# Kernel optimization log

Measured on AMD Instinct MI355X. Metric: run time of the kernel, lower is better.

The kernel has to match this reference:

```python
import jax, jax.numpy as jnp
import numpy as np

B_, T_, IN_, H_, N_ = 16, 4096, 2, 256, 256
TWO_PI = 6.283185307179586


def setup_inputs() -> dict:
    key = jax.random.key(0)
    ks = jax.random.split(key, 12)
    x = jax.random.normal(ks[0], (B_, T_, IN_), dtype=jnp.float32)
    lengths = jax.random.randint(ks[1], (B_,), 1, T_ + 1)  # in [1, T]
    # canonical LRU param init (ring init for eigenvalues)
    u1 = jax.random.uniform(ks[2], (N_,))
    u2 = jax.random.uniform(ks[3], (N_,))
    nu_log = jnp.log(-0.5 * jnp.log(u1 * 0.75 + 0.25))          # |lam| in [0.5, 1)
    theta_log = jnp.log(u2 * TWO_PI + 1e-4)
    B_re = jax.random.normal(ks[4], (N_, IN_)) / np.sqrt(2 * IN_)
    B_im = jax.random.normal(ks[5], (N_, IN_)) / np.sqrt(2 * IN_)
    C_re = jax.random.normal(ks[6], (H_, N_)) / np.sqrt(N_)
    C_im = jax.random.normal(ks[7], (H_, N_)) / np.sqrt(N_)
    D = jax.random.normal(ks[8], (H_, IN_))
    Wh = jax.random.normal(ks[9], (1, H_)) / np.sqrt(H_)
    bh = jnp.zeros((1,), dtype=jnp.float32)
    return {"x": x, "lengths": lengths, "nu_log": nu_log.astype(jnp.float32),
            "theta_log": theta_log.astype(jnp.float32), "B_re": B_re.astype(jnp.float32),
            "B_im": B_im.astype(jnp.float32), "C_re": C_re.astype(jnp.float32),
            "C_im": C_im.astype(jnp.float32), "D": D.astype(jnp.float32),
            "Wh": Wh.astype(jnp.float32), "bh": bh}


def _combine(e1, e2):
    a1, b1 = e1
    a2, b2 = e2
    return a1 * a2, a2 * b1 + b2


def reference(x, lengths, nu_log, theta_log, B_re, B_im, C_re, C_im, D, Wh, bh):
    B, T, _ = x.shape
    lam = jnp.exp(-jnp.exp(nu_log) + 1j * jnp.exp(theta_log))          # [N] complex
    gamma = jnp.sqrt(1.0 - jnp.abs(lam) ** 2)                           # [N] real
    Bmat = (B_re + 1j * B_im) * gamma[:, None]                          # [N, IN]
    Bu = jnp.einsum('bti,ni->btn', x.astype(jnp.complex64), Bmat)       # [B,T,N]
    a = jnp.broadcast_to(lam.astype(jnp.complex64), Bu.shape)
    # parallel associative scan of x_t = lam*x_{t-1} + Bu_t along time
    _, states = jax.lax.associative_scan(_combine, (a, Bu), axis=1)     # [B,T,N]
    C = C_re + 1j * C_im                                                # [H,N]
    y = jnp.einsum('btn,hn->bth', states, C).real + x @ D.T             # [B,T,H]
    mask = (jnp.arange(T) < lengths[:, None])[..., None]                # [B,T,1]
    y = y * mask
    last = jnp.take_along_axis(y, (lengths - 1)[:, None, None], axis=1)[:, 0, :]  # [B,H]
    return last @ Wh.T + bh                                             # [B,1]
```

## Files before the change

kernel.cpp:

```cpp
#include <hip/hip_runtime.h>
#include <hip/hip_bf16.h>

#define B_ 16
#define T_ 4096
#define IN_ 2
#define H_ 256
#define N_ 256

#define TWO_PI_F 6.28318530717958647692f
#define INV_TWO_PI_D 0.15915494309189533576888376337251

__global__ __launch_bounds__(256) void cw_kernel(const float* __restrict__ C_re,
                                                 const float* __restrict__ C_im,
                                                 const float* __restrict__ Wh,
                                                 float2* __restrict__ Cw) {
    int n = blockIdx.x;
    int h = threadIdx.x;
    float w = Wh[h];
    float vr = w * C_re[h * N_ + n];
    float vi = w * C_im[h * N_ + n];
    for (int off = 32; off > 0; off >>= 1) {
        vr += __shfl_down(vr, off);
        vi += __shfl_down(vi, off);
    }
    __shared__ float2 sred[4];
    int wid = threadIdx.x >> 6;
    int lane = threadIdx.x & 63;
    if (lane == 0) sred[wid] = make_float2(vr, vi);
    __syncthreads();
    if (threadIdx.x == 0) {
        float2 t = sred[0];
        t.x += sred[1].x + sred[2].x + sred[3].x;
        t.y += sred[1].y + sred[2].y + sred[3].y;
        Cw[n] = t;
    }
}

__global__ __launch_bounds__(256) void lru_state_kernel(
        const float* __restrict__ x, const int* __restrict__ lengths,
        const float* __restrict__ nu_log, const float* __restrict__ theta_log,
        const float* __restrict__ B_re, const float* __restrict__ B_im,
        const float2* __restrict__ Cw, float* __restrict__ g) {
    const int n = blockIdx.x;
    const int b = blockIdx.y;
    const int L = lengths[b];
    const int tstar = L - 1;

    const float nu = __expf(nu_log[n]);
    const float th = __expf(theta_log[n]);
    const double threv = (double)th * INV_TWO_PI_D;

    const float2* xb = ((const float2*)x) + (size_t)b * T_;

    float a0r = 0.f, a0i = 0.f, a1r = 0.f, a1i = 0.f;
    for (int s = threadIdx.x; s < L; s += 256) {
        int k = tstar - s;
        double f = (double)k * threv;
        float r = (float)(f - rint(f));
        float ang = r * TWO_PI_F;
        float sn, cs;
        __sincosf(ang, &sn, &cs);
        float e = __expf(-(float)k * nu);
        float vr = e * cs;
        float vi = e * sn;
        float2 xv = xb[s];
        a0r = fmaf(vr, xv.x, a0r);
        a0i = fmaf(vi, xv.x, a0i);
        a1r = fmaf(vr, xv.y, a1r);
        a1i = fmaf(vi, xv.y, a1i);
    }

    for (int off = 32; off > 0; off >>= 1) {
        a0r += __shfl_down(a0r, off);
        a0i += __shfl_down(a0i, off);
        a1r += __shfl_down(a1r, off);
        a1i += __shfl_down(a1i, off);
    }
    __shared__ float4 sred[4];
    int wid = threadIdx.x >> 6;
    int lane = threadIdx.x & 63;
    if (lane == 0) sred[wid] = make_float4(a0r, a0i, a1r, a1i);
    __syncthreads();
    if (threadIdx.x == 0) {
        float4 t = sred[0];
        t.x += sred[1].x + sred[2].x + sred[3].x;
        t.y += sred[1].y + sred[2].y + sred[3].y;
        t.z += sred[1].z + sred[2].z + sred[3].z;
        t.w += sred[1].w + sred[2].w + sred[3].w;
        float gamma = sqrtf(1.f - __expf(-2.f * nu));
        float br0 = B_re[2 * n] * gamma, bi0 = B_im[2 * n] * gamma;
        float br1 = B_re[2 * n + 1] * gamma, bi1 = B_im[2 * n + 1] * gamma;
        float str = t.x * br0 - t.y * bi0 + t.z * br1 - t.w * bi1;
        float sti = t.x * bi0 + t.y * br0 + t.z * bi1 + t.w * br1;
        float2 cw = Cw[n];
        g[b * N_ + n] = str * cw.x - sti * cw.y;
    }
}

__global__ __launch_bounds__(256) void out_kernel(
        const float* __restrict__ g, const float* __restrict__ x,
        const int* __restrict__ lengths, const float* __restrict__ D,
        const float* __restrict__ Wh, const float* __restrict__ bh,
        float* __restrict__ out) {
    int b = blockIdx.x;
    int tstar = lengths[b] - 1;
    int h = threadIdx.x;
    float2 xv = ((const float2*)x)[(size_t)b * T_ + tstar];
    float v = g[b * N_ + h] + Wh[h] * (D[2 * h] * xv.x + D[2 * h + 1] * xv.y);
    for (int off = 32; off > 0; off >>= 1) v += __shfl_down(v, off);
    __shared__ float sred[4];
    int wid = threadIdx.x >> 6;
    int lane = threadIdx.x & 63;
    if (lane == 0) sred[wid] = v;
    __syncthreads();
    if (threadIdx.x == 0) {
        out[b] = sred[0] + sred[1] + sred[2] + sred[3] + bh[0];
    }
}

extern "C" void kernel_launch(void* const* d_in, const int* in_sizes, int n_in,
                              void* d_out, int out_size, void* d_ws, size_t ws_size,
                              hipStream_t stream) {
    const float* x         = (const float*)d_in[0];
    const int*   lengths   = (const int*)d_in[1];
    const float* nu_log    = (const float*)d_in[2];
    const float* theta_log = (const float*)d_in[3];
    const float* B_re      = (const float*)d_in[4];
    const float* B_im      = (const float*)d_in[5];
    const float* C_re      = (const float*)d_in[6];
    const float* C_im      = (const float*)d_in[7];
    const float* D         = (const float*)d_in[8];
    const float* Wh        = (const float*)d_in[9];
    const float* bh        = (const float*)d_in[10];
    float* out = (float*)d_out;

    float2* Cw = (float2*)d_ws;
    float*  g  = (float*)d_ws + 2 * N_;

    cw_kernel<<<N_, 256, 0, stream>>>(C_re, C_im, Wh, Cw);
    lru_state_kernel<<<dim3(N_, B_), 256, 0, stream>>>(x, lengths, nu_log, theta_log,
                                                       B_re, B_im, Cw, g);
    out_kernel<<<B_, 256, 0, stream>>>(g, x, lengths, D, Wh, bh, out);
}
```

Baseline: 86.70 us.

## Replace per-step sincos/exp with a complex power recurrence and fuse the output kernel

Each thread now evaluates sincos and exp only twice: once for its starting power lam^k0 and once for the stride factor lam^256. It then advances the power by complex multiplication instead of recomputing the double-precision angle reduction, sincos and exp on every timestep. The output reduction kernel is removed: the D term and bias are written by an extended setup kernel, and each state block adds its contribution to out with an atomic add, saving one launch. The costs are rounding error that accumulates through the recurrence (about 16 steps per thread), order-dependent float atomics, and a dependence on setup_kernel writing out before lru_kernel runs.

```diff
diff --git a/kernel.cpp b/kernel.cpp
--- a/kernel.cpp
+++ b/kernel.cpp
@@ -10,41 +10,57 @@
 #define TWO_PI_F 6.28318530717958647692f
 #define INV_TWO_PI_D 0.15915494309189533576888376337251
 
-__global__ __launch_bounds__(256) void cw_kernel(const float* __restrict__ C_re,
-                                                 const float* __restrict__ C_im,
-                                                 const float* __restrict__ Wh,
-                                                 float2* __restrict__ Cw) {
-    int n = blockIdx.x;
+__global__ __launch_bounds__(256) void setup_kernel(
+        const float* __restrict__ C_re, const float* __restrict__ C_im,
+        const float* __restrict__ Wh, const float* __restrict__ bh,
+        const float* __restrict__ D, const float* __restrict__ x,
+        const int* __restrict__ lengths,
+        float2* __restrict__ Cw, float* __restrict__ out) {
+    __shared__ float2 sred[4];
     int h = threadIdx.x;
-    float w = Wh[h];
-    float vr = w * C_re[h * N_ + n];
-    float vi = w * C_im[h * N_ + n];
-    for (int off = 32; off > 0; off >>= 1) {
-        vr += __shfl_down(vr, off);
-        vi += __shfl_down(vi, off);
-    }
-    __shared__ float2 sred[4];
     int wid = threadIdx.x >> 6;
     int lane = threadIdx.x & 63;
-    if (lane == 0) sred[wid] = make_float2(vr, vi);
-    __syncthreads();
-    if (threadIdx.x == 0) {
-        float2 t = sred[0];
-        t.x += sred[1].x + sred[2].x + sred[3].x;
-        t.y += sred[1].y + sred[2].y + sred[3].y;
-        Cw[n] = t;
+    float w = Wh[h];
+
+    if (blockIdx.x < N_) {
+        int n = blockIdx.x;
+        float vr = w * C_re[h * N_ + n];
+        float vi = w * C_im[h * N_ + n];
+        for (int off = 32; off > 0; off >>= 1) {
+            vr += __shfl_down(vr, off);
+            vi += __shfl_down(vi, off);
+        }
+        if (lane == 0) sred[wid] = make_float2(vr, vi);
+        __syncthreads();
+        if (threadIdx.x == 0) {
+            float2 t = sred[0];
+            t.x += sred[1].x + sred[2].x + sred[3].x;
+            t.y += sred[1].y + sred[2].y + sred[3].y;
+            Cw[n] = t;
+        }
+    } else {
+        int b = blockIdx.x - N_;
+        int tstar = lengths[b] - 1;
+        float2 xv = ((const float2*)x)[(size_t)b * T_ + tstar];
+        float v = w * (D[2 * h] * xv.x + D[2 * h + 1] * xv.y);
+        for (int off = 32; off > 0; off >>= 1) v += __shfl_down(v, off);
+        if (lane == 0) sred[wid] = make_float2(v, 0.f);
+        __syncthreads();
+        if (threadIdx.x == 0) {
+            out[b] = sred[0].x + sred[1].x + sred[2].x + sred[3].x + bh[0];
+        }
     }
 }
 
-__global__ __launch_bounds__(256) void lru_state_kernel(
+__global__ __launch_bounds__(256) void lru_kernel(
         const float* __restrict__ x, const int* __restrict__ lengths,
         const float* __restrict__ nu_log, const float* __restrict__ theta_log,
         const float* __restrict__ B_re, const float* __restrict__ B_im,
-        const float2* __restrict__ Cw, float* __restrict__ g) {
+        const float2* __restrict__ Cw, float* __restrict__ out) {
     const int n = blockIdx.x;
     const int b = blockIdx.y;
-    const int L = lengths[b];
-    const int tstar = L - 1;
+    const int tid = threadIdx.x;
+    const int tstar = lengths[b] - 1;
 
     const float nu = __expf(nu_log[n]);
     const float th = __expf(theta_log[n]);
@@ -53,21 +69,32 @@
     const float2* xb = ((const float2*)x) + (size_t)b * T_;
 
     float a0r = 0.f, a0i = 0.f, a1r = 0.f, a1i = 0.f;
-    for (int s = threadIdx.x; s < L; s += 256) {
-        int k = tstar - s;
-        double f = (double)k * threv;
-        float r = (float)(f - rint(f));
-        float ang = r * TWO_PI_F;
+    if (tid <= tstar) {
+        const int k0 = (tstar - tid) & 255;
+        const int s0 = tstar - k0;
+        double f0 = (double)k0 * threv;
+        float ang0 = (float)(f0 - rint(f0)) * TWO_PI_F;
         float sn, cs;
-        __sincosf(ang, &sn, &cs);
-        float e = __expf(-(float)k * nu);
-        float vr = e * cs;
-        float vi = e * sn;
-        float2 xv = xb[s];
-        a0r = fmaf(vr, xv.x, a0r);
-        a0i = fmaf(vi, xv.x, a0i);
-        a1r = fmaf(vr, xv.y, a1r);
-        a1i = fmaf(vi, xv.y, a1i);
+        __sincosf(ang0, &sn, &cs);
+        float e0 = __expf(-(float)k0 * nu);
+        float fr = e0 * cs, fi = e0 * sn;
+        double f2 = 256.0 * threv;
+        float ang2 = (float)(f2 - rint(f2)) * TWO_PI_F;
+        __sincosf(ang2, &sn, &cs);
+        float e2 = __expf(-256.f * nu);
+        float rr = e2 * cs, ri = e2 * sn;
+
+        for (int s = s0; s >= 0; s -= 256) {
+            float2 xv = xb[s];
+            a0r = fmaf(fr, xv.x, a0r);
+            a0i = fmaf(fi, xv.x, a0i);
+            a1r = fmaf(fr, xv.y, a1r);
+            a1i = fmaf(fi, xv.y, a1i);
+            float nfr = fr * rr - fi * ri;
+            float nfi = fmaf(fr, ri, fi * rr);
+            fr = nfr;
+            fi = nfi;
+        }
     }
 
     for (int off = 32; off > 0; off >>= 1) {
@@ -93,28 +120,8 @@
         float str = t.x * br0 - t.y * bi0 + t.z * br1 - t.w * bi1;
         float sti = t.x * bi0 + t.y * br0 + t.z * bi1 + t.w * br1;
         float2 cw = Cw[n];
-        g[b * N_ + n] = str * cw.x - sti * cw.y;
-    }
-}
-
-__global__ __launch_bounds__(256) void out_kernel(
-        const float* __restrict__ g, const float* __restrict__ x,
-        const int* __restrict__ lengths, const float* __restrict__ D,
-        const float* __restrict__ Wh, const float* __restrict__ bh,
-        float* __restrict__ out) {
-    int b = blockIdx.x;
-    int tstar = lengths[b] - 1;
-    int h = threadIdx.x;
-    float2 xv = ((const float2*)x)[(size_t)b * T_ + tstar];
-    float v = g[b * N_ + h] + Wh[h] * (D[2 * h] * xv.x + D[2 * h + 1] * xv.y);
-    for (int off = 32; off > 0; off >>= 1) v += __shfl_down(v, off);
-    __shared__ float sred[4];
-    int wid = threadIdx.x >> 6;
-    int lane = threadIdx.x & 63;
-    if (lane == 0) sred[wid] = v;
-    __syncthreads();
-    if (threadIdx.x == 0) {
-        out[b] = sred[0] + sred[1] + sred[2] + sred[3] + bh[0];
+        float gval = str * cw.x - sti * cw.y;
+        unsafeAtomicAdd(&out[b], gval);
     }
 }
 
@@ -135,10 +142,9 @@
     float* out = (float*)d_out;
 
     float2* Cw = (float2*)d_ws;
-    float*  g  = (float*)d_ws + 2 * N_;
 
-    cw_kernel<<<N_, 256, 0, stream>>>(C_re, C_im, Wh, Cw);
-    lru_state_kernel<<<dim3(N_, B_), 256, 0, stream>>>(x, lengths, nu_log, theta_log,
-                                                       B_re, B_im, Cw, g);
-    out_kernel<<<B_, 256, 0, stream>>>(g, x, lengths, D, Wh, bh, out);
+    setup_kernel<<<N_ + B_, 256, 0, stream>>>(C_re, C_im, Wh, bh, D, x, lengths,
+                                              Cw, out);
+    lru_kernel<<<dim3(N_, B_), 256, 0, stream>>>(x, lengths, nu_log, theta_log,
+                                                 B_re, B_im, Cw, out);
 }
```

New measurement: 131.9 us. 52.2% more time.
